# Kernel tuning notes

Hardware: AMD Instinct MI355X
Metric: run time of the kernel (lower is better)

Reference implementation:

```python
import jax, jax.numpy as jnp
import numpy as np

B, H, L = 4096, 1024, 4


def _lstm_cell(x, h, c, Wih, Whh, bih, bhh):
    # gates: [B, 4H], PyTorch gate order i, f, g, o
    gates = x @ Wih.T + bih + h @ Whh.T + bhh
    i, f, g, o = jnp.split(gates, 4, axis=-1)
    i = jax.nn.sigmoid(i)
    f = jax.nn.sigmoid(f)
    g = jnp.tanh(g)
    o = jax.nn.sigmoid(o)
    c2 = f * c + i * g
    h2 = o * jnp.tanh(c2)
    return h2, c2


def setup_inputs() -> dict:
    key = jax.random.key(0)
    ks = jax.random.split(key, 7)
    scale = 1.0 / np.sqrt(H)  # PyTorch LSTMCell init range
    return {
        "x": jax.random.normal(ks[0], (B, H), jnp.float32),
        "h0": jax.random.normal(ks[1], (B, H, L), jnp.float32),
        "c0": jax.random.normal(ks[2], (B, H, L), jnp.float32),
        "W_ih": jax.random.normal(ks[3], (L, 4 * H, H), jnp.float32) * scale,
        "W_hh": jax.random.normal(ks[4], (L, 4 * H, H), jnp.float32) * scale,
        "b_ih": jax.random.normal(ks[5], (L, 4 * H), jnp.float32) * scale,
        "b_hh": jax.random.normal(ks[6], (L, 4 * H), jnp.float32) * scale,
    }


def reference(x, h0, c0, W_ih, W_hh, b_ih, b_hh):
    # Multi-layer LSTM cell: layer i consumes the hidden output of layer i-1
    # (dropout=None -> identity between layers). prev states indexed on last dim.
    lstm_input = x
    hs, cs = [], []
    for i in range(L):
        h_i, c_i = _lstm_cell(lstm_input, h0[:, :, i], c0[:, :, i],
                              W_ih[i], W_hh[i], b_ih[i], b_hh[i])
        lstm_input = h_i
        hs.append(h_i)
        cs.append(c_i)
    # torch.stack -> [L, B, H]; permute(1, 2, 0) -> [B, H, L]
    next_hidden = jnp.stack(hs, axis=-1)
    next_cell = jnp.stack(cs, axis=-1)
    return next_hidden, next_cell
```

## Files before the change

### kernel.cpp

```cpp
#include <hip/hip_runtime.h>
#include <cstddef>

#define BATCH 4096
#define HID   1024
#define NLAY  4
#define NG    4096
#define KTOT  2048

typedef short short8 __attribute__((ext_vector_type(8)));
typedef float f32x4  __attribute__((ext_vector_type(4)));

__device__ __forceinline__ unsigned short f2bf(float f) {
    union { float f; unsigned u; } v; v.f = f;
    unsigned r = v.u + 0x7fffu + ((v.u >> 16) & 1u);
    return (unsigned short)(r >> 16);
}

__device__ __forceinline__ float sigm_f(float x) {
    return 1.0f / (1.0f + __expf(-x));
}
__device__ __forceinline__ float tanh_f(float x) {
    float e = __expf(-2.0f * fabsf(x));
    float r = (1.0f - e) / (1.0f + e);
    return copysignf(r, x);
}

#define GLOAD_LDS16(g, l)                                                            \
    __builtin_amdgcn_global_load_lds(                                                \
        (const __attribute__((address_space(1))) void*)(g),                          \
        (__attribute__((address_space(3))) void*)(l), 16, 0, 0)

__global__ __launch_bounds__(256) void prep_weights(
    const float* __restrict__ Wih, const float* __restrict__ Whh,
    unsigned short* __restrict__ Wb)
{
    size_t t    = (size_t)blockIdx.x * 256 + threadIdx.x;
    size_t base = t * 4;
    size_t row  = base >> 11;
    int    k    = (int)(base & (KTOT - 1));
    const float* src = (k < HID) ? (Wih + row * HID + k)
                                 : (Whh + row * HID + (k - HID));
    float4 v = *(const float4*)src;
    ushort4 o; o.x = f2bf(v.x); o.y = f2bf(v.y); o.z = f2bf(v.z); o.w = f2bf(v.w);
    *(ushort4*)(Wb + base) = o;
}

__global__ __launch_bounds__(256) void prep_bias(
    const float* __restrict__ bih, const float* __restrict__ bhh,
    float* __restrict__ bias)
{
    int i = blockIdx.x * 256 + threadIdx.x;
    bias[i] = bih[i] + bhh[i];
}

__global__ __launch_bounds__(256) void prep_A(
    const float* __restrict__ x, const float* __restrict__ h0,
    unsigned short* __restrict__ A0, unsigned short* __restrict__ A1,
    unsigned short* __restrict__ A2, unsigned short* __restrict__ A3)
{
    int idx = blockIdx.x * 256 + threadIdx.x;
    int b = idx >> 10, h = idx & (HID - 1);
    float4 hv = *(const float4*)(h0 + (size_t)idx * NLAY);
    A0[(size_t)b * KTOT + h]       = f2bf(x[idx]);
    A0[(size_t)b * KTOT + HID + h] = f2bf(hv.x);
    A1[(size_t)b * KTOT + HID + h] = f2bf(hv.y);
    A2[(size_t)b * KTOT + HID + h] = f2bf(hv.z);
    A3[(size_t)b * KTOT + HID + h] = f2bf(hv.w);
}

__global__ __launch_bounds__(256, 2) void gemm_lstm_fused(
    const unsigned short* __restrict__ A,
    const unsigned short* __restrict__ W,
    const float* __restrict__ bias,
    const float* __restrict__ c0,
    float* __restrict__ outH,
    float* __restrict__ outC,
    unsigned short* __restrict__ Anext,
    int layer)
{
    __shared__ unsigned short ldsA[128 * 64];
    __shared__ unsigned short ldsB[128 * 64];

    const int tid  = threadIdx.x;
    const int wave = tid >> 6;
    const int lane = tid & 63;
    const int bn = blockIdx.x, bm = blockIdx.y;
    const int wm = wave >> 1, wn = wave & 1;

    f32x4 acc[4][4] = {};

    const int srow8 = lane >> 3;
    const int scol  = (lane & 7) * 8;
    const unsigned short* Ag = A + (size_t)(bm * 128 + wave * 32 + srow8) * KTOT + scol;
    const unsigned short* Wg[4];
#pragma unroll
    for (int j = 0; j < 4; ++j) {
        int s    = wave * 32 + j * 8 + srow8;
        int wrow = ((s >> 4) & 3) * HID + bn * 32 + (s >> 6) * 16 + (s & 15);
        Wg[j] = W + (size_t)wrow * KTOT + scol;
    }

    const int lrd = (lane & 15) * 64 + (lane >> 4) * 8;

    for (int k0 = 0; k0 < KTOT; k0 += 64) {
#pragma unroll
        for (int j = 0; j < 4; ++j) {
            GLOAD_LDS16(Ag + (size_t)(j * 8) * KTOT + k0, &ldsA[(wave * 32 + j * 8) * 64]);
            GLOAD_LDS16(Wg[j] + k0,                        &ldsB[(wave * 32 + j * 8) * 64]);
        }
        __syncthreads();
#pragma unroll
        for (int kk = 0; kk < 2; ++kk) {
            short8 af[4], bf[4];
#pragma unroll
            for (int m = 0; m < 4; ++m)
                af[m] = *(const short8*)&ldsA[(wm * 64 + m * 16) * 64 + lrd + kk * 32];
#pragma unroll
            for (int n = 0; n < 4; ++n)
                bf[n] = *(const short8*)&ldsB[(wn * 64 + n * 16) * 64 + lrd + kk * 32];
#pragma unroll
            for (int m = 0; m < 4; ++m)
#pragma unroll
                for (int n = 0; n < 4; ++n)
                    acc[m][n] = __builtin_amdgcn_mfma_f32_16x16x32_bf16(
                        af[m], bf[n], acc[m][n], 0, 0, 0);
        }
        __syncthreads();
    }

    const int h = bn * 32 + wn * 16 + (lane & 15);
    float bv[4];
#pragma unroll
    for (int n = 0; n < 4; ++n) bv[n] = bias[n * HID + h];

#pragma unroll
    for (int m = 0; m < 4; ++m) {
        const int b0 = bm * 128 + wm * 64 + m * 16 + ((lane >> 4) << 2);
#pragma unroll
        for (int r = 0; r < 4; ++r) {
            const int b = b0 + r;
            const size_t oi = ((size_t)b * HID + h) * NLAY + layer;
            float iv = sigm_f(acc[m][0][r] + bv[0]);
            float fv = sigm_f(acc[m][1][r] + bv[1]);
            float gv = tanh_f(acc[m][2][r] + bv[2]);
            float ov = sigm_f(acc[m][3][r] + bv[3]);
            float c2 = fv * c0[oi] + iv * gv;
            float h2 = ov * tanh_f(c2);
            outH[oi] = h2;
            outC[oi] = c2;
            if (Anext) Anext[(size_t)b * KTOT + h] = f2bf(h2);
        }
    }
}

extern "C" void kernel_launch(void* const* d_in, const int* in_sizes, int n_in,
                              void* d_out, int out_size, void* d_ws, size_t ws_size,
                              hipStream_t stream)
{
    const float* x   = (const float*)d_in[0];
    const float* h0  = (const float*)d_in[1];
    const float* c0  = (const float*)d_in[2];
    const float* Wih = (const float*)d_in[3];
    const float* Whh = (const float*)d_in[4];
    const float* bih = (const float*)d_in[5];
    const float* bhh = (const float*)d_in[6];

    float* outH = (float*)d_out;
    float* outC = outH + (size_t)BATCH * HID * NLAY;

    char* ws = (char*)d_ws;
    unsigned short* Wb   = (unsigned short*)(ws);
    float*          bias = (float*)(ws + 67108864);
    unsigned short* Ap[4];
    Ap[0] = (unsigned short*)(ws + 67174400);
    Ap[1] = (unsigned short*)(ws + 83951616);
    Ap[2] = (unsigned short*)(ws + 100728832);
    Ap[3] = (unsigned short*)(ws + 117506048);

    prep_weights<<<32768, 256, 0, stream>>>(Wih, Whh, Wb);
    prep_bias<<<64, 256, 0, stream>>>(bih, bhh, bias);
    prep_A<<<BATCH * HID / 256, 256, 0, stream>>>(x, h0, Ap[0], Ap[1], Ap[2], Ap[3]);

    for (int l = 0; l < NLAY; ++l) {
        gemm_lstm_fused<<<dim3(HID / 32, BATCH / 128), 256, 0, stream>>>(
            Ap[l], Wb + (size_t)l * NG * KTOT, bias + l * NG, c0,
            outH, outC, (l < NLAY - 1) ? Ap[l + 1] : nullptr, l);
    }
}
```

Measured before the change: 774.3 us.

## XOR-swizzle LDS tiles and stage cell/hidden states in layer-major buffers

```diff
diff --git a/kernel.cpp b/kernel.cpp
--- a/kernel.cpp
+++ b/kernel.cpp
@@ -6,6 +6,7 @@
 #define NLAY  4
 #define NG    4096
 #define KTOT  2048
+#define BH    (BATCH * HID)
 
 typedef short short8 __attribute__((ext_vector_type(8)));
 typedef float f32x4  __attribute__((ext_vector_type(4)));
@@ -53,10 +54,12 @@
     bias[i] = bih[i] + bhh[i];
 }
 
-__global__ __launch_bounds__(256) void prep_A(
+__global__ __launch_bounds__(256) void prep_misc(
     const float* __restrict__ x, const float* __restrict__ h0,
+    const float* __restrict__ c0,
     unsigned short* __restrict__ A0, unsigned short* __restrict__ A1,
-    unsigned short* __restrict__ A2, unsigned short* __restrict__ A3)
+    unsigned short* __restrict__ A2, unsigned short* __restrict__ A3,
+    float* __restrict__ cc)
 {
     int idx = blockIdx.x * 256 + threadIdx.x;
     int b = idx >> 10, h = idx & (HID - 1);
@@ -66,15 +69,23 @@
     A1[(size_t)b * KTOT + HID + h] = f2bf(hv.y);
     A2[(size_t)b * KTOT + HID + h] = f2bf(hv.z);
     A3[(size_t)b * KTOT + HID + h] = f2bf(hv.w);
-}
-
+    if (cc) {
+        float4 cv = *(const float4*)(c0 + (size_t)idx * NLAY);
+        cc[idx]          = cv.x;
+        cc[BH + idx]     = cv.y;
+        cc[2 * BH + idx] = cv.z;
+        cc[3 * BH + idx] = cv.w;
+    }
+}
+
+template<bool LM>
 __global__ __launch_bounds__(256, 2) void gemm_lstm_fused(
     const unsigned short* __restrict__ A,
     const unsigned short* __restrict__ W,
     const float* __restrict__ bias,
-    const float* __restrict__ c0,
-    float* __restrict__ outH,
-    float* __restrict__ outC,
+    const float* cin,
+    float* cout,
+    float* __restrict__ hout,
     unsigned short* __restrict__ Anext,
     int layer)
 {
@@ -90,7 +101,7 @@
     f32x4 acc[4][4] = {};
 
     const int srow8 = lane >> 3;
-    const int scol  = (lane & 7) * 8;
+    const int scol  = (((lane & 7) ^ srow8) << 3);
     const unsigned short* Ag = A + (size_t)(bm * 128 + wave * 32 + srow8) * KTOT + scol;
     const unsigned short* Wg[4];
 #pragma unroll
@@ -100,7 +111,8 @@
         Wg[j] = W + (size_t)wrow * KTOT + scol;
     }
 
-    const int lrd = (lane & 15) * 64 + (lane >> 4) * 8;
+    const int rrow = lane & 15;
+    const int rkey = lane & 7;
 
     for (int k0 = 0; k0 < KTOT; k0 += 64) {
 #pragma unroll
@@ -111,13 +123,14 @@
         __syncthreads();
 #pragma unroll
         for (int kk = 0; kk < 2; ++kk) {
+            const int ro = ((((lane >> 4) + kk * 4) ^ rkey) << 3);
             short8 af[4], bf[4];
 #pragma unroll
             for (int m = 0; m < 4; ++m)
-                af[m] = *(const short8*)&ldsA[(wm * 64 + m * 16) * 64 + lrd + kk * 32];
+                af[m] = *(const short8*)&ldsA[(wm * 64 + m * 16 + rrow) * 64 + ro];
 #pragma unroll
             for (int n = 0; n < 4; ++n)
-                bf[n] = *(const short8*)&ldsB[(wn * 64 + n * 16) * 64 + lrd + kk * 32];
+                bf[n] = *(const short8*)&ldsB[(wn * 64 + n * 16 + rrow) * 64 + ro];
 #pragma unroll
             for (int m = 0; m < 4; ++m)
 #pragma unroll
@@ -139,18 +152,30 @@
 #pragma unroll
         for (int r = 0; r < 4; ++r) {
             const int b = b0 + r;
-            const size_t oi = ((size_t)b * HID + h) * NLAY + layer;
+            const size_t idx2 = LM ? ((size_t)b * HID + h)
+                                   : (((size_t)b * HID + h) * NLAY + layer);
             float iv = sigm_f(acc[m][0][r] + bv[0]);
             float fv = sigm_f(acc[m][1][r] + bv[1]);
             float gv = tanh_f(acc[m][2][r] + bv[2]);
             float ov = sigm_f(acc[m][3][r] + bv[3]);
-            float c2 = fv * c0[oi] + iv * gv;
+            float c2 = fv * cin[idx2] + iv * gv;
             float h2 = ov * tanh_f(c2);
-            outH[oi] = h2;
-            outC[oi] = c2;
+            cout[idx2] = c2;
+            hout[idx2] = h2;
             if (Anext) Anext[(size_t)b * KTOT + h] = f2bf(h2);
         }
     }
+}
+
+__global__ __launch_bounds__(256) void interleave(
+    const float* __restrict__ hT, const float* __restrict__ cc,
+    float* __restrict__ outH, float* __restrict__ outC)
+{
+    int idx = blockIdx.x * 256 + threadIdx.x;
+    float4 hv = { hT[idx], hT[BH + idx], hT[2 * BH + idx], hT[3 * BH + idx] };
+    float4 cv = { cc[idx], cc[BH + idx], cc[2 * BH + idx], cc[3 * BH + idx] };
+    *(float4*)(outH + (size_t)idx * NLAY) = hv;
+    *(float4*)(outC + (size_t)idx * NLAY) = cv;
 }
 
 extern "C" void kernel_launch(void* const* d_in, const int* in_sizes, int n_in,
@@ -166,7 +191,7 @@
     const float* bhh = (const float*)d_in[6];
 
     float* outH = (float*)d_out;
-    float* outC = outH + (size_t)BATCH * HID * NLAY;
+    float* outC = outH + (size_t)BH * NLAY;
 
     char* ws = (char*)d_ws;
     unsigned short* Wb   = (unsigned short*)(ws);
@@ -177,13 +202,29 @@
     Ap[2] = (unsigned short*)(ws + 100728832);
     Ap[3] = (unsigned short*)(ws + 117506048);
 
+    const bool lm = (ws_size >= 268500992ULL);
+    float* cc = lm ? (float*)(ws + 134283264) : nullptr;
+    float* hT = lm ? (float*)(ws + 201392128) : nullptr;
+
     prep_weights<<<32768, 256, 0, stream>>>(Wih, Whh, Wb);
     prep_bias<<<64, 256, 0, stream>>>(bih, bhh, bias);
-    prep_A<<<BATCH * HID / 256, 256, 0, stream>>>(x, h0, Ap[0], Ap[1], Ap[2], Ap[3]);
-
+    prep_misc<<<BH / 256, 256, 0, stream>>>(x, h0, c0,
+                                            Ap[0], Ap[1], Ap[2], Ap[3], cc);
+
+    const dim3 grid(HID / 32, BATCH / 128);
     for (int l = 0; l < NLAY; ++l) {
-        gemm_lstm_fused<<<dim3(HID / 32, BATCH / 128), 256, 0, stream>>>(
-            Ap[l], Wb + (size_t)l * NG * KTOT, bias + l * NG, c0,
-            outH, outC, (l < NLAY - 1) ? Ap[l + 1] : nullptr, l);
-    }
-}
+        unsigned short* An = (l < NLAY - 1) ? Ap[l + 1] : nullptr;
+        const unsigned short* Wl = Wb + (size_t)l * NG * KTOT;
+        const float* bl = bias + l * NG;
+        if (lm) {
+            gemm_lstm_fused<true><<<grid, 256, 0, stream>>>(
+                Ap[l], Wl, bl, cc + (size_t)l * BH, cc + (size_t)l * BH,
+                hT + (size_t)l * BH, An, l);
+        } else {
+            gemm_lstm_fused<false><<<grid, 256, 0, stream>>>(
+                Ap[l], Wl, bl, c0, outC, outH, An, l);
+        }
+    }
+
+    if (lm) interleave<<<BH / 256, 256, 0, stream>>>(hT, cc, outH, outC);
+}
```

Result: faster. 683.1 us (-11.8%).
